# Kernel tuning notes

Measured on AMD Instinct MI355X. Metric: run time of the kernel, lower is better.

## Reference

```python
import jax, jax.numpy as jnp
import numpy as np

# Static problem sizes (uniform graphs for jit-friendliness)
B = 64          # number of hypergraphs in the batch
N_PER = 32      # shape-nodes per hypergraph (num_nodes_hgraph, uniform)
D_ID = 256      # shape_id_dim
D_MULT = 64     # shape_multiplicity_dim
LATENT = 512    # latent_dim
D_NODE = D_ID + D_MULT           # 320
FEAT = 3 * D_NODE + LATENT       # 1472, MLP input dim
HID = 2 * FEAT                   # 2944
NUM_ATOMS = 11                   # 1 + feature_sizes['num_atoms']
VOCAB_ID, VOCAB_MULT = 100, 20


def setup_inputs() -> dict:
    key = jax.random.key(0)
    ks = jax.random.split(key, 11)
    s1 = 1.0 / np.sqrt(FEAT)
    s2 = 1.0 / np.sqrt(HID)
    s3 = 1.0 / np.sqrt(FEAT)
    return {
        "shape_node_idx": jax.random.randint(ks[0], (B * N_PER,), 0, VOCAB_ID),
        "shape_node_mult": jax.random.randint(ks[1], (B * N_PER,), 0, VOCAB_MULT),
        "z_graph": jax.random.normal(ks[2], (B, LATENT), jnp.float32),
        "id_emb": jax.random.normal(ks[3], (VOCAB_ID, D_ID), jnp.float32) * 0.02,
        "mult_emb": jax.random.normal(ks[4], (VOCAB_MULT, D_MULT), jnp.float32) * 0.02,
        "W1": jax.random.normal(ks[5], (FEAT, HID), jnp.float32) * s1,
        "b1": jnp.zeros((HID,), jnp.float32),
        "W2": jax.random.normal(ks[6], (HID, FEAT), jnp.float32) * s2,
        "b2": jnp.zeros((FEAT,), jnp.float32),
        "W3": jax.random.normal(ks[7], (FEAT, NUM_ATOMS), jnp.float32) * s3,
        "b3": jnp.zeros((NUM_ATOMS,), jnp.float32),
    }


def reference(shape_node_idx, shape_node_mult, z_graph, id_emb, mult_emb,
              W1, b1, W2, b2, W3, b3):
    # Node features: concat of shape-id and multiplicity embeddings -> [B, n, d_node]
    x = jnp.concatenate([id_emb[shape_node_idx], mult_emb[shape_node_mult]], axis=-1)
    x = x.reshape(B, N_PER, D_NODE)

    # Per-graph segment aggregation (node_aggregation='mean') -> [B, d_node]
    agg = x.mean(axis=1)

    # All intra-graph node pairs (block-diagonal edge pattern), edge (i, j):
    # input = [x_i, x_j, z_graph, agg] broadcast to [B, n, n, FEAT]
    xi = jnp.broadcast_to(x[:, :, None, :], (B, N_PER, N_PER, D_NODE))
    xj = jnp.broadcast_to(x[:, None, :, :], (B, N_PER, N_PER, D_NODE))
    zg = jnp.broadcast_to(z_graph[:, None, None, :], (B, N_PER, N_PER, LATENT))
    ag = jnp.broadcast_to(agg[:, None, None, :], (B, N_PER, N_PER, D_NODE))
    feat = jnp.concatenate([xi, xj, zg, ag], axis=-1)  # [B, n, n, FEAT]

    # MLP [FEAT, 2*FEAT, FEAT, NUM_ATOMS] with ReLU activations
    h = jax.nn.relu(jnp.einsum('bijf,fh->bijh', feat, W1) + b1)
    h = jax.nn.relu(jnp.einsum('bijh,hf->bijf', h, W2) + b2)
    logits = jnp.einsum('bijf,fa->bija', h, W3) + b3  # [B, n, n, A]

    # _to_symmetric: average each edge value with its transpose
    logits = 0.5 * (logits + jnp.swapaxes(logits, 1, 2))

    # Flattened per-edge logits (matches sparse COO value order: row-major pairs)
    return logits.reshape(B * N_PER * N_PER, NUM_ATOMS)
```

## Files before the change

kernel.cpp:

```cpp
#include <hip/hip_runtime.h>
#include <stdint.h>

#define NBG   64
#define NPER  32
#define DNODE 320
#define FEAT  1472
#define HIDN  2944
#define FEATP 1536
#define NA    11
#define NROWS 2048
#define MEDGE 65536

typedef __attribute__((ext_vector_type(8))) short    bf16x8;
typedef __attribute__((ext_vector_type(4))) float    fv4;
typedef __attribute__((ext_vector_type(2))) float    fv2;
typedef __attribute__((ext_vector_type(4))) unsigned uiv4;

__device__ __forceinline__ unsigned short f2bf(float f) {
  unsigned u = __builtin_bit_cast(unsigned, f);
  u += 0x7fffu + ((u >> 16) & 1u);
  return (unsigned short)(u >> 16);
}
__device__ __forceinline__ float bf2f(unsigned short h) {
  unsigned u = ((unsigned)h) << 16;
  return __builtin_bit_cast(float, u);
}
__device__ __forceinline__ unsigned cvt_pk_bf16(float lo, float hi) {
  unsigned r;
  asm("v_cvt_pk_bf16_f32 %0, %1, %2" : "=v"(r) : "v"(lo), "v"(hi));
  return r;
}
__device__ __forceinline__ fv2 pk_add(fv2 a, fv2 b) {
  fv2 d;
  asm("v_pk_add_f32 %0, %1, %2" : "=v"(d) : "v"(a), "v"(b));
  return d;
}
__device__ __forceinline__ unsigned pk_relu2(unsigned x, unsigned z) {
  unsigned r;
  asm("v_pk_max_i16 %0, %1, %2" : "=v"(r) : "v"(x), "v"(z));
  return r;
}
__device__ __forceinline__ fv2 lo2(fv4 v) { return __builtin_shufflevector(v, v, 0, 1); }
__device__ __forceinline__ fv2 hi2(fv4 v) { return __builtin_shufflevector(v, v, 2, 3); }
__device__ __forceinline__ void gload_lds16(const void* g, void* l) {
  __builtin_amdgcn_global_load_lds((const __attribute__((address_space(1))) void*)g,
                                   (__attribute__((address_space(3))) void*)l, 16, 0, 0);
}

__global__ void k_transpose_bf16(const float* __restrict__ src, unsigned short* __restrict__ dst,
                                 int K, int N, int Npad) {
  __shared__ float tile[64][65];
  int k0 = blockIdx.x * 64, n0 = blockIdx.y * 64;
  int r = threadIdx.x >> 2, cb = (threadIdx.x & 3) * 16;
  const float* srow = src + (size_t)(k0 + r) * N + n0 + cb;
#pragma unroll
  for (int c = 0; c < 16; ++c) {
    int n = n0 + cb + c;
    tile[r][cb + c] = (n < N) ? srow[c] : 0.f;
  }
  __syncthreads();
  unsigned short* drow = dst + (size_t)(n0 + r) * K + k0 + cb;
#pragma unroll
  for (int c = 0; c < 16; ++c) drow[c] = f2bf(tile[cb + c][r]);
}

__global__ void k_embed(const int* __restrict__ idx, const int* __restrict__ mlt,
                        const float* __restrict__ id_emb, const float* __restrict__ mult_emb,
                        unsigned short* __restrict__ xb) {
  int t = blockIdx.x, c = threadIdx.x;
  int iv = idx[t], mv = mlt[t];
  xb[t * DNODE + c] = f2bf(id_emb[iv * 256 + c]);
  if (c < 64) xb[t * DNODE + 256 + c] = f2bf(mult_emb[mv * 64 + c]);
}

__global__ void k_agg(const unsigned short* __restrict__ xb, float* __restrict__ agg) {
  int b = blockIdx.x;
  for (int d = threadIdx.x; d < DNODE; d += 256) {
    float s = 0.f;
    for (int i = 0; i < NPER; ++i) s += bf2f(xb[(b * NPER + i) * DNODE + d]);
    agg[b * DNODE + d] = s * (1.f / 32.f);
  }
}

__global__ void k_za(const float* __restrict__ z, const float* __restrict__ agg,
                     unsigned short* __restrict__ za) {
  int b = blockIdx.x;
  for (int c = threadIdx.x; c < 832; c += 256) {
    unsigned short v = 0;
    if (b < NBG) v = (c < 512) ? f2bf(z[b * 512 + c]) : f2bf(agg[b * DNODE + (c - 512)]);
    za[b * 832 + c] = v;
  }
}

__global__ void k_gemm1(const unsigned short* __restrict__ A, int sA, int Mrows,
                        const unsigned short* __restrict__ W1T, int kOff, int Ksteps,
                        float* __restrict__ C, const float* __restrict__ bias) {
  __shared__ alignas(16) unsigned short Als[128 * 32];
  __shared__ alignas(16) unsigned short Bls[128 * 32];
  int bx = blockIdx.x;
  int mt = bx / 23, nc = bx - mt * 23;
  int m0 = mt * 128, n0 = nc * 128;
  int tid = threadIdx.x, lane = tid & 63, w = tid >> 6;

  fv4 acc[4][4] = {};
  for (int kt = 0; kt < Ksteps; ++kt) {
    int k0 = kt * 32;
    __syncthreads();
#pragma unroll
    for (int q = 0; q < 2; ++q) {
      int seg = w * 2 + q;
      int row = seg * 16 + (lane >> 2);
      int col = (lane & 3) * 8;
      gload_lds16(A + (size_t)(m0 + row) * sA + k0 + col, &Als[seg * 512]);
      gload_lds16(W1T + (size_t)(n0 + row) * FEAT + kOff + k0 + col, &Bls[seg * 512]);
    }
    __syncthreads();
    bf16x8 aF[4], bF[4];
#pragma unroll
    for (int mf = 0; mf < 4; ++mf)
      aF[mf] = *(const bf16x8*)&Als[((w >> 1) * 64 + mf * 16 + (lane & 15)) * 32 + (lane >> 4) * 8];
#pragma unroll
    for (int nf = 0; nf < 4; ++nf)
      bF[nf] = *(const bf16x8*)&Bls[((w & 1) * 64 + nf * 16 + (lane & 15)) * 32 + (lane >> 4) * 8];
#pragma unroll
    for (int mf = 0; mf < 4; ++mf)
#pragma unroll
      for (int nf = 0; nf < 4; ++nf)
        acc[mf][nf] = __builtin_amdgcn_mfma_f32_16x16x32_bf16(aF[mf], bF[nf], acc[mf][nf], 0, 0, 0);
  }
  int mq = (w >> 1) * 64, nq = (w & 1) * 64;
#pragma unroll
  for (int mf = 0; mf < 4; ++mf)
#pragma unroll
    for (int nf = 0; nf < 4; ++nf) {
      int n = n0 + nq + nf * 16 + (lane & 15);
      float bv = bias ? bias[n] : 0.f;
#pragma unroll
      for (int r = 0; r < 4; ++r) {
        int m = m0 + mq + mf * 16 + (lane >> 4) * 4 + r;
        if (m < Mrows) C[(size_t)m * HIDN + n] = acc[mf][nf][r] + bv;
      }
    }
}

__global__ void k_pq(float* __restrict__ P1, const float* __restrict__ Q) {
  int r = blockIdx.x;
  const float* q = Q + (size_t)(r >> 5) * HIDN;
  float* p = P1 + (size_t)r * HIDN;
  for (int n = threadIdx.x; n < HIDN; n += 256) p[n] += q[n];
}

__global__ void k_zero(float* __restrict__ p, int n) {
  int i = blockIdx.x * 256 + threadIdx.x;
  if (i < n) p[i] = 0.f;
}

__global__ __launch_bounds__(256, 2)
void k_gemm2(const float* __restrict__ PQ1, const float* __restrict__ P2,
             const unsigned short* __restrict__ W2T,
             const float* __restrict__ b2, const float* __restrict__ W3,
             float* __restrict__ Lout) {
  __shared__ alignas(16) unsigned char LB[43008];
  int raw = blockIdx.x;
  int bx = (raw & 7) * 384 + (raw >> 3);
  int mt = bx / 6, nc2 = bx - mt * 6;
  int m0 = mt * 128, n0 = nc2 * 256;
  int tid = threadIdx.x, lane = tid & 63, w = tid >> 6;
  int bG = m0 >> 10;
  int i0 = (m0 >> 5) & 31;
  int ks = lane >> 4;
  int r  = lane & 15;

  const int swcolB = ((lane & 3) ^ ((lane >> 3) & 3)) * 8;
  const int swcolP = (((lane >> 1) & 3) ^ ((lane >> 3) & 3)) * 8 + (lane & 1) * 4;

  auto STAGEB = [&](int kt, int buf) {
#pragma unroll
    for (int q = 0; q < 4; ++q) {
      int seg = w * 4 + q;
      int row = seg * 16 + (lane >> 2);
      gload_lds16(W2T + (size_t)(n0 + row) * HIDN + kt * 32 + swcolB,
                  LB + buf * 16384 + seg * 1024);
    }
  };
  auto STAGESRC = [&](int kt, int buf) {
    gload_lds16(P2 + (size_t)(bG * NPER + 8 * w + (lane >> 3)) * HIDN + kt * 32 + swcolP,
                LB + 32768 + buf * 4096 + w * 1024);
    if (w == 0)
      gload_lds16(PQ1 + (size_t)(bG * NPER + i0 + (lane >> 3)) * HIDN + kt * 32 + (lane & 7) * 4,
                  LB + 40960 + buf * 1024);
  };

  fv4 acc[4][8] = {};
  unsigned z0 = 0;
  asm volatile("" : "+v"(z0));

  STAGEB(0, 0);
  STAGESRC(0, 0);
  __syncthreads();

  int il0 = (w >> 1) * 2;
  for (int kt = 0; kt < 92; ++kt) {
    int cur = kt & 1, nxt = cur ^ 1;
    if (kt < 91) { STAGEB(kt + 1, nxt); STAGESRC(kt + 1, nxt); }

    const unsigned char* Bb = LB + cur * 16384;
    const unsigned char* Pb = LB + 32768 + cur * 4096;
    const unsigned char* Qb = LB + 40960 + cur * 1024;

    int psw = (ks ^ (r & 3)) * 32;
    fv4 q0[2], q1[2], p0[2], p1[2];
#pragma unroll
    for (int h = 0; h < 2; ++h) {
      q0[h] = *(const fv4*)(Qb + il0 * 128 + ks * 32 + h * 16);
      q1[h] = *(const fv4*)(Qb + (il0 + 1) * 128 + ks * 32 + h * 16);
      p0[h] = *(const fv4*)(Pb + r * 128 + psw + h * 16);
      p1[h] = *(const fv4*)(Pb + (16 + r) * 128 + psw + h * 16);
    }
    bf16x8 bF[8];
#pragma unroll
    for (int nf = 0; nf < 8; ++nf) {
      int brow = (w & 1) * 128 + nf * 16 + r;
      int slot = ks ^ ((brow >> 1) & 3);
      bF[nf] = *(const bf16x8*)(Bb + brow * 64 + slot * 16);
    }

    bf16x8 aF[4];
#pragma unroll
    for (int mf = 0; mf < 4; ++mf) {
      fv4 qa0 = (mf & 2) ? q1[0] : q0[0];
      fv4 qa1 = (mf & 2) ? q1[1] : q0[1];
      fv4 pa0 = (mf & 1) ? p1[0] : p0[0];
      fv4 pa1 = (mf & 1) ? p1[1] : p0[1];
      fv2 s00 = pk_add(lo2(qa0), lo2(pa0));
      fv2 s01 = pk_add(hi2(qa0), hi2(pa0));
      fv2 s10 = pk_add(lo2(qa1), lo2(pa1));
      fv2 s11 = pk_add(hi2(qa1), hi2(pa1));
      uiv4 u;
      u[0] = pk_relu2(cvt_pk_bf16(s00[0], s00[1]), z0);
      u[1] = pk_relu2(cvt_pk_bf16(s01[0], s01[1]), z0);
      u[2] = pk_relu2(cvt_pk_bf16(s10[0], s10[1]), z0);
      u[3] = pk_relu2(cvt_pk_bf16(s11[0], s11[1]), z0);
      aF[mf] = __builtin_bit_cast(bf16x8, u);
    }

#pragma unroll
    for (int nf = 0; nf < 8; ++nf)
#pragma unroll
      for (int mf = 0; mf < 4; ++mf)
        acc[mf][nf] = __builtin_amdgcn_mfma_f32_16x16x32_bf16(aF[mf], bF[nf], acc[mf][nf], 0, 0, 0);
    __syncthreads();
  }

  float* red = (float*)LB;
  int nq = (w & 1) * 128;
#pragma unroll
  for (int mf = 0; mf < 4; ++mf) {
    float s[4][NA];
#pragma unroll
    for (int rr = 0; rr < 4; ++rr)
#pragma unroll
      for (int a = 0; a < NA; ++a) s[rr][a] = 0.f;
#pragma unroll
    for (int nf = 0; nf < 8; ++nf) {
      int n = n0 + nq + nf * 16 + r;
      if (n < FEAT) {
        float bv = b2[n];
        float w3r[NA];
#pragma unroll
        for (int a = 0; a < NA; ++a) w3r[a] = W3[n * NA + a];
#pragma unroll
        for (int rr = 0; rr < 4; ++rr) {
          float h = fmaxf(acc[mf][nf][rr] + bv, 0.f);
#pragma unroll
          for (int a = 0; a < NA; ++a) s[rr][a] += h * w3r[a];
        }
      }
    }
#pragma unroll
    for (int off = 1; off < 16; off <<= 1)
#pragma unroll
      for (int rr = 0; rr < 4; ++rr)
#pragma unroll
        for (int a = 0; a < NA; ++a) s[rr][a] += __shfl_xor(s[rr][a], off, 64);
    int a = r;
    if (a < NA) {
#pragma unroll
      for (int rr = 0; rr < 4; ++rr)
        red[w * 704 + (mf * 16 + ks * 4 + rr) * NA + a] = s[rr][a];
    }
  }
  __syncthreads();
  for (int e = tid; e < 128 * NA; e += 256) {
    int row = e / NA, a = e - row * NA;
    int wr = row >> 6, rr = row & 63;
    float v = red[(wr * 2 + 0) * 704 + rr * NA + a] + red[(wr * 2 + 1) * 704 + rr * NA + a];
    atomicAdd(&Lout[(size_t)(m0 + row) * NA + a], v);
  }
}

__global__ void k_sym(const float* __restrict__ Lraw, const float* __restrict__ b3,
                      float* __restrict__ out) {
  int e = blockIdx.x * 256 + threadIdx.x;
  if (e >= MEDGE * NA) return;
  int m = e / NA, a = e - m * NA;
  int msw = (m & ~1023) | ((m & 31) << 5) | ((m >> 5) & 31);
  out[e] = 0.5f * (Lraw[e] + Lraw[(size_t)msw * NA + a]) + b3[a];
}

extern "C" void kernel_launch(void* const* d_in, const int* in_sizes, int n_in,
                              void* d_out, int out_size, void* d_ws, size_t ws_size,
                              hipStream_t stream) {
  const int*   idx      = (const int*)d_in[0];
  const int*   mlt      = (const int*)d_in[1];
  const float* z        = (const float*)d_in[2];
  const float* id_emb   = (const float*)d_in[3];
  const float* mult_emb = (const float*)d_in[4];
  const float* W1       = (const float*)d_in[5];
  const float* b1       = (const float*)d_in[6];
  const float* W2       = (const float*)d_in[7];
  const float* b2       = (const float*)d_in[8];
  const float* W3       = (const float*)d_in[9];
  const float* b3       = (const float*)d_in[10];
  float* out = (float*)d_out;

  uint8_t* ws = (uint8_t*)d_ws;
  size_t o = 0;
  auto alloc = [&](size_t bytes) { size_t r = o; o += (bytes + 255) & ~(size_t)255; return r; };
  size_t oW1T = alloc((size_t)HIDN * FEAT * 2);
  size_t oW2T = alloc((size_t)FEATP * HIDN * 2);
  size_t oXB  = alloc((size_t)NROWS * DNODE * 2);
  size_t oZA  = alloc((size_t)128 * 832 * 2);
  size_t oAG  = alloc((size_t)NBG * DNODE * 4);
  size_t oP1  = alloc((size_t)NROWS * HIDN * 4);
  size_t oP2  = alloc((size_t)NROWS * HIDN * 4);
  size_t oQ   = alloc((size_t)NBG * HIDN * 4);
  size_t oLR  = alloc((size_t)MEDGE * NA * 4);
  if (ws_size < o) return;

  unsigned short* W1T = (unsigned short*)(ws + oW1T);
  unsigned short* W2T = (unsigned short*)(ws + oW2T);
  unsigned short* xb  = (unsigned short*)(ws + oXB);
  unsigned short* za  = (unsigned short*)(ws + oZA);
  float* agg = (float*)(ws + oAG);
  float* P1  = (float*)(ws + oP1);
  float* P2  = (float*)(ws + oP2);
  float* Qm  = (float*)(ws + oQ);
  float* LR  = (float*)(ws + oLR);

  k_transpose_bf16<<<dim3(FEAT / 64, HIDN / 64), 256, 0, stream>>>(W1, W1T, FEAT, HIDN, HIDN);
  k_transpose_bf16<<<dim3(HIDN / 64, FEATP / 64), 256, 0, stream>>>(W2, W2T, HIDN, FEAT, FEATP);
  k_embed<<<NROWS, 256, 0, stream>>>(idx, mlt, id_emb, mult_emb, xb);
  k_agg<<<NBG, 256, 0, stream>>>(xb, agg);
  k_za<<<128, 256, 0, stream>>>(z, agg, za);
  k_gemm1<<<16 * 23, 256, 0, stream>>>(xb, DNODE, NROWS, W1T, 0, 10, P1, nullptr);
  k_gemm1<<<16 * 23, 256, 0, stream>>>(xb, DNODE, NROWS, W1T, 320, 10, P2, nullptr);
  k_gemm1<<<1 * 23, 256, 0, stream>>>(za, 832, NBG, W1T, 640, 26, Qm, b1);
  k_pq<<<NROWS, 256, 0, stream>>>(P1, Qm);
  k_zero<<<(MEDGE * NA + 255) / 256, 256, 0, stream>>>(LR, MEDGE * NA);
  k_gemm2<<<512 * 6, 256, 0, stream>>>(P1, P2, W2T, b2, W3, LR);
  k_sym<<<(MEDGE * NA + 255) / 256, 256, 0, stream>>>(LR, b3, out);
}
```

Baseline: 1.144 ms.

## Deepen gemm2 LDS pipeline to four B stages with two k-steps per barrier

Restructures the k-loop of the second GEMM kernel to process two k-tiles per iteration. It uses four W2T buffers, three rotating P2 buffers, and combined Q loads, and keeps prefetches two k-steps ahead. This halves the number of full __syncthreads and gives global-to-LDS loads more time to land before use. The cost is raising LDS per block from ~42KB to ~78KB, which may cap occupancy below the 2 blocks per CU the launch bounds ask for, and adds buffer-index bookkeeping.

```diff
diff --git a/kernel.cpp b/kernel.cpp
--- a/kernel.cpp
+++ b/kernel.cpp
@@ -160,53 +160,49 @@
              const unsigned short* __restrict__ W2T,
              const float* __restrict__ b2, const float* __restrict__ W3,
              float* __restrict__ Lout) {
-  __shared__ alignas(16) unsigned char LB[43008];
+  __shared__ alignas(16) unsigned char LB[79872];
   int raw = blockIdx.x;
   int bx = (raw & 7) * 384 + (raw >> 3);
   int mt = bx / 6, nc2 = bx - mt * 6;
   int m0 = mt * 128, n0 = nc2 * 256;
-  int tid = threadIdx.x, lane = tid & 63, w = tid >> 6;
+  int tid = threadIdx.x, lane = tid & 63, wv = tid >> 6;
   int bG = m0 >> 10;
   int i0 = (m0 >> 5) & 31;
   int ks = lane >> 4;
   int r  = lane & 15;
+  int il0 = (wv >> 1) * 2;
 
   const int swcolB = ((lane & 3) ^ ((lane >> 3) & 3)) * 8;
   const int swcolP = (((lane >> 1) & 3) ^ ((lane >> 3) & 3)) * 8 + (lane & 1) * 4;
 
-  auto STAGEB = [&](int kt, int buf) {
+  auto STAGEB = [&](int t, int buf) {
 #pragma unroll
     for (int q = 0; q < 4; ++q) {
-      int seg = w * 4 + q;
+      int seg = wv * 4 + q;
       int row = seg * 16 + (lane >> 2);
-      gload_lds16(W2T + (size_t)(n0 + row) * HIDN + kt * 32 + swcolB,
+      gload_lds16(W2T + (size_t)(n0 + row) * HIDN + t * 32 + swcolB,
                   LB + buf * 16384 + seg * 1024);
     }
   };
-  auto STAGESRC = [&](int kt, int buf) {
-    gload_lds16(P2 + (size_t)(bG * NPER + 8 * w + (lane >> 3)) * HIDN + kt * 32 + swcolP,
-                LB + 32768 + buf * 4096 + w * 1024);
-    if (w == 0)
-      gload_lds16(PQ1 + (size_t)(bG * NPER + i0 + (lane >> 3)) * HIDN + kt * 32 + (lane & 7) * 4,
-                  LB + 40960 + buf * 1024);
+  auto STAGEP = [&](int t, int buf) {
+    gload_lds16(P2 + (size_t)(bG * NPER + 8 * wv + (lane >> 3)) * HIDN + t * 32 + swcolP,
+                LB + 65536 + buf * 4096 + wv * 1024);
+  };
+  auto STAGEQ = [&](int t2, int qb) {
+    if (wv == 0)
+      gload_lds16(PQ1 + (size_t)(bG * NPER + i0 + ((lane >> 3) & 3)) * HIDN
+                      + (t2 + (lane >> 5)) * 32 + (lane & 7) * 4,
+                  LB + 77824 + qb * 512);
   };
 
   fv4 acc[4][8] = {};
   unsigned z0 = 0;
   asm volatile("" : "+v"(z0));
 
-  STAGEB(0, 0);
-  STAGESRC(0, 0);
-  __syncthreads();
-
-  int il0 = (w >> 1) * 2;
-  for (int kt = 0; kt < 92; ++kt) {
-    int cur = kt & 1, nxt = cur ^ 1;
-    if (kt < 91) { STAGEB(kt + 1, nxt); STAGESRC(kt + 1, nxt); }
-
-    const unsigned char* Bb = LB + cur * 16384;
-    const unsigned char* Pb = LB + 32768 + cur * 4096;
-    const unsigned char* Qb = LB + 40960 + cur * 1024;
+  auto BODY = [&](int bB, int bP, int bQ) {
+    const unsigned char* Bb = LB + bB * 16384;
+    const unsigned char* Pb = LB + 65536 + bP * 4096;
+    const unsigned char* Qb = LB + 77824 + bQ * 512;
 
     int psw = (ks ^ (r & 3)) * 32;
     fv4 q0[2], q1[2], p0[2], p1[2];
@@ -220,7 +216,7 @@
     bf16x8 bF[8];
 #pragma unroll
     for (int nf = 0; nf < 8; ++nf) {
-      int brow = (w & 1) * 128 + nf * 16 + r;
+      int brow = (wv & 1) * 128 + nf * 16 + r;
       int slot = ks ^ ((brow >> 1) & 3);
       bF[nf] = *(const bf16x8*)(Bb + brow * 64 + slot * 16);
     }
@@ -249,11 +245,41 @@
 #pragma unroll
       for (int mf = 0; mf < 4; ++mf)
         acc[mf][nf] = __builtin_amdgcn_mfma_f32_16x16x32_bf16(aF[mf], bF[nf], acc[mf][nf], 0, 0, 0);
+  };
+
+  STAGEB(0, 0); STAGEB(1, 1);
+  STAGEP(0, 0); STAGEP(1, 1);
+  STAGEQ(0, 0);
+  __syncthreads();
+
+  int p0i = 0, b0i = 0;
+  for (int wi = 0; wi < 46; ++wi) {
+    int p1i = p0i + 1; if (p1i == 3) p1i = 0;
+    int p2i = p1i + 1; if (p2i == 3) p2i = 0;
+    int t0 = 2 * wi;
+
+    if (wi < 45) {
+      STAGEB(t0 + 2, b0i ^ 2);
+      STAGEB(t0 + 3, b0i ^ 3);
+      STAGEP(t0 + 2, p2i);
+      STAGEQ(t0 + 2, b0i ^ 2);
+    }
+
+    BODY(b0i, p0i, b0i);
+
+    asm volatile("s_waitcnt lgkmcnt(0)" ::: "memory");
+    __builtin_amdgcn_s_barrier();
+
+    if (wi < 45) STAGEP(t0 + 3, p0i);
+
+    BODY(b0i ^ 1, p1i, b0i ^ 1);
+
     __syncthreads();
+    p0i = p2i; b0i ^= 2;
   }
 
   float* red = (float*)LB;
-  int nq = (w & 1) * 128;
+  int nq = (wv & 1) * 128;
 #pragma unroll
   for (int mf = 0; mf < 4; ++mf) {
     float s[4][NA];
@@ -287,7 +313,7 @@
     if (a < NA) {
 #pragma unroll
       for (int rr = 0; rr < 4; ++rr)
-        red[w * 704 + (mf * 16 + ks * 4 + rr) * NA + a] = s[rr][a];
+        red[wv * 704 + (mf * 16 + ks * 4 + rr) * NA + a] = s[rr][a];
     }
   }
   __syncthreads();
```

Measured after the change: 1.202 ms. +5.0%, slower.

## Halve gemm2 M-tile to 64 rows to raise occupancy to three blocks

Applied to the files above, without the earlier changes.

The second fused GEMM now uses 64-row M tiles, so each block covers two i-rows instead of four. That halves the accumulator registers and shrinks LDS, which allows launch_bounds of 3 blocks per CU, and the grid doubles. The cost is that each W2T B-tile is now reused across half as many rows, so the W2 tile traffic from L2/LDS per FLOP doubles and the number of atomic adds rises.

```diff
diff --git a/kernel.cpp b/kernel.cpp
--- a/kernel.cpp
+++ b/kernel.cpp
@@ -155,19 +155,21 @@
   if (i < n) p[i] = 0.f;
 }
 
-__global__ __launch_bounds__(256, 2)
+__global__ __launch_bounds__(256, 3)
 void k_gemm2(const float* __restrict__ PQ1, const float* __restrict__ P2,
              const unsigned short* __restrict__ W2T,
              const float* __restrict__ b2, const float* __restrict__ W3,
              float* __restrict__ Lout) {
-  __shared__ alignas(16) unsigned char LB[43008];
+  __shared__ alignas(16) unsigned char LB[41472];
   int raw = blockIdx.x;
-  int bx = (raw & 7) * 384 + (raw >> 3);
-  int mt = bx / 6, nc2 = bx - mt * 6;
-  int m0 = mt * 128, n0 = nc2 * 256;
+  int g = (raw & 7) * 768 + (raw >> 3);
+  int nc2 = g / 1024;
+  int mt  = g - nc2 * 1024;
+  int m0 = mt * 64, n0 = nc2 * 256;
   int tid = threadIdx.x, lane = tid & 63, w = tid >> 6;
   int bG = m0 >> 10;
   int i0 = (m0 >> 5) & 31;
+  int iw = w >> 1;
   int ks = lane >> 4;
   int r  = lane & 15;
 
@@ -186,12 +188,12 @@
   auto STAGESRC = [&](int kt, int buf) {
     gload_lds16(P2 + (size_t)(bG * NPER + 8 * w + (lane >> 3)) * HIDN + kt * 32 + swcolP,
                 LB + 32768 + buf * 4096 + w * 1024);
-    if (w == 0)
+    if (w == 0 && lane < 16)
       gload_lds16(PQ1 + (size_t)(bG * NPER + i0 + (lane >> 3)) * HIDN + kt * 32 + (lane & 7) * 4,
-                  LB + 40960 + buf * 1024);
+                  LB + 40960 + buf * 256);
   };
 
-  fv4 acc[4][8] = {};
+  fv4 acc[2][8] = {};
   unsigned z0 = 0;
   asm volatile("" : "+v"(z0));
 
@@ -199,21 +201,19 @@
   STAGESRC(0, 0);
   __syncthreads();
 
-  int il0 = (w >> 1) * 2;
   for (int kt = 0; kt < 92; ++kt) {
     int cur = kt & 1, nxt = cur ^ 1;
     if (kt < 91) { STAGEB(kt + 1, nxt); STAGESRC(kt + 1, nxt); }
 
     const unsigned char* Bb = LB + cur * 16384;
     const unsigned char* Pb = LB + 32768 + cur * 4096;
-    const unsigned char* Qb = LB + 40960 + cur * 1024;
+    const unsigned char* Qb = LB + 40960 + cur * 256;
 
     int psw = (ks ^ (r & 3)) * 32;
-    fv4 q0[2], q1[2], p0[2], p1[2];
+    fv4 q0[2], p0[2], p1[2];
 #pragma unroll
     for (int h = 0; h < 2; ++h) {
-      q0[h] = *(const fv4*)(Qb + il0 * 128 + ks * 32 + h * 16);
-      q1[h] = *(const fv4*)(Qb + (il0 + 1) * 128 + ks * 32 + h * 16);
+      q0[h] = *(const fv4*)(Qb + iw * 128 + ks * 32 + h * 16);
       p0[h] = *(const fv4*)(Pb + r * 128 + psw + h * 16);
       p1[h] = *(const fv4*)(Pb + (16 + r) * 128 + psw + h * 16);
     }
@@ -225,17 +225,15 @@
       bF[nf] = *(const bf16x8*)(Bb + brow * 64 + slot * 16);
     }
 
-    bf16x8 aF[4];
-#pragma unroll
-    for (int mf = 0; mf < 4; ++mf) {
-      fv4 qa0 = (mf & 2) ? q1[0] : q0[0];
-      fv4 qa1 = (mf & 2) ? q1[1] : q0[1];
-      fv4 pa0 = (mf & 1) ? p1[0] : p0[0];
-      fv4 pa1 = (mf & 1) ? p1[1] : p0[1];
-      fv2 s00 = pk_add(lo2(qa0), lo2(pa0));
-      fv2 s01 = pk_add(hi2(qa0), hi2(pa0));
-      fv2 s10 = pk_add(lo2(qa1), lo2(pa1));
-      fv2 s11 = pk_add(hi2(qa1), hi2(pa1));
+    bf16x8 aF[2];
+#pragma unroll
+    for (int mf = 0; mf < 2; ++mf) {
+      fv4 pa0 = mf ? p1[0] : p0[0];
+      fv4 pa1 = mf ? p1[1] : p0[1];
+      fv2 s00 = pk_add(lo2(q0[0]), lo2(pa0));
+      fv2 s01 = pk_add(hi2(q0[0]), hi2(pa0));
+      fv2 s10 = pk_add(lo2(q0[1]), lo2(pa1));
+      fv2 s11 = pk_add(hi2(q0[1]), hi2(pa1));
       uiv4 u;
       u[0] = pk_relu2(cvt_pk_bf16(s00[0], s00[1]), z0);
       u[1] = pk_relu2(cvt_pk_bf16(s01[0], s01[1]), z0);
@@ -247,7 +245,7 @@
 #pragma unroll
     for (int nf = 0; nf < 8; ++nf)
 #pragma unroll
-      for (int mf = 0; mf < 4; ++mf)
+      for (int mf = 0; mf < 2; ++mf)
         acc[mf][nf] = __builtin_amdgcn_mfma_f32_16x16x32_bf16(aF[mf], bF[nf], acc[mf][nf], 0, 0, 0);
     __syncthreads();
   }
@@ -255,7 +253,7 @@
   float* red = (float*)LB;
   int nq = (w & 1) * 128;
 #pragma unroll
-  for (int mf = 0; mf < 4; ++mf) {
+  for (int mf = 0; mf < 2; ++mf) {
     float s[4][NA];
 #pragma unroll
     for (int rr = 0; rr < 4; ++rr)
@@ -287,14 +285,14 @@
     if (a < NA) {
 #pragma unroll
       for (int rr = 0; rr < 4; ++rr)
-        red[w * 704 + (mf * 16 + ks * 4 + rr) * NA + a] = s[rr][a];
+        red[w * 352 + (mf * 16 + ks * 4 + rr) * NA + a] = s[rr][a];
     }
   }
   __syncthreads();
-  for (int e = tid; e < 128 * NA; e += 256) {
+  for (int e = tid; e < 64 * NA; e += 256) {
     int row = e / NA, a = e - row * NA;
-    int wr = row >> 6, rr = row & 63;
-    float v = red[(wr * 2 + 0) * 704 + rr * NA + a] + red[(wr * 2 + 1) * 704 + rr * NA + a];
+    int ri = row >> 5, l = row & 31;
+    float v = red[(ri * 2 + 0) * 352 + l * NA + a] + red[(ri * 2 + 1) * 352 + l * NA + a];
     atomicAdd(&Lout[(size_t)(m0 + row) * NA + a], v);
   }
 }
@@ -358,6 +356,6 @@
   k_gemm1<<<1 * 23, 256, 0, stream>>>(za, 832, NBG, W1T, 640, 26, Qm, b1);
   k_pq<<<NROWS, 256, 0, stream>>>(P1, Qm);
   k_zero<<<(MEDGE * NA + 255) / 256, 256, 0, stream>>>(LR, MEDGE * NA);
-  k_gemm2<<<512 * 6, 256, 0, stream>>>(P1, P2, W2T, b2, W3, LR);
+  k_gemm2<<<1024 * 6, 256, 0, stream>>>(P1, P2, W2T, b2, W3, LR);
   k_sym<<<(MEDGE * NA + 255) / 256, 256, 0, stream>>>(LR, b3, out);
 }
```

Measured after the change: 1.358 ms. 18.6% more time.
